# Kernel optimization log

Measured on AMD Instinct MI355X. Metric: run time of the kernel, lower is better.

The kernel has to match this reference:

```python
import jax, jax.numpy as jnp
import numpy as np

B, S, D, H = 4, 2048, 1024, 16
DK = D // H

def setup_inputs() -> dict:
    key = jax.random.key(0)
    ks = jax.random.split(key, 11)
    s = 1.0 / np.sqrt(D)
    return {
        "query": jax.random.normal(ks[0], (B, S, D), jnp.float32),
        "key_": jax.random.normal(ks[1], (B, S, D), jnp.float32),
        "value": jax.random.normal(ks[2], (B, S, D), jnp.float32),
        "Wq": jax.random.uniform(ks[3], (D, D), jnp.float32, -s, s),
        "bq": jax.random.uniform(ks[4], (D,), jnp.float32, -s, s),
        "Wk": jax.random.uniform(ks[5], (D, D), jnp.float32, -s, s),
        "bk": jax.random.uniform(ks[6], (D,), jnp.float32, -s, s),
        "Wv": jax.random.uniform(ks[7], (D, D), jnp.float32, -s, s),
        "bv": jax.random.uniform(ks[8], (D,), jnp.float32, -s, s),
        "Wo": jax.random.uniform(ks[9], (D, D), jnp.float32, -s, s),
        "bo": jax.random.uniform(ks[10], (D,), jnp.float32, -s, s),
    }

def _split_heads(x):
    # [B,S,D] -> [B,H,S,DK]
    b, s, _ = x.shape
    return x.reshape(b, s, H, DK).transpose(0, 2, 1, 3)

def reference(query, key_, value, Wq, bq, Wk, bk, Wv, bv, Wo, bo):
    Q = _split_heads(query @ Wq.T + bq)
    K = _split_heads(key_ @ Wk.T + bk)
    V = _split_heads(value @ Wv.T + bv)
    scores = jnp.einsum('bhqd,bhkd->bhqk', Q, K) / np.sqrt(DK).astype(np.float32)
    attn = jax.nn.softmax(scores, axis=-1)
    ctx = jnp.einsum('bhqk,bhkd->bhqd', attn, V)  # [B,H,S,DK]
    ctx = ctx.transpose(0, 2, 1, 3).reshape(query.shape[0], -1, D)
    return ctx @ Wo.T + bo
```

## Files before the change

kernel.cpp:

```cpp
#include <hip/hip_runtime.h>
#include <hip/hip_bf16.h>
#include <math.h>


#define B_SZ   4
#define S_LEN  2048
#define D_DIM  1024
#define NH     16
#define DKD    64
#define M_TOT  (B_SZ * S_LEN)

typedef __bf16 bf16_t;
typedef bf16_t bf16x8 __attribute__((ext_vector_type(8)));
typedef bf16_t bf16x4 __attribute__((ext_vector_type(4)));
typedef float  f32x4  __attribute__((ext_vector_type(4)));

typedef __attribute__((address_space(1))) void gvoid;
typedef __attribute__((address_space(3))) void lvoid;

extern "C" __device__ float __ocml_native_exp2_f32(float);

__global__ __launch_bounds__(256)
void cvt3_kernel(const float* __restrict__ s0, const float* __restrict__ s1,
                 const float* __restrict__ s2, bf16_t* __restrict__ d0,
                 bf16_t* __restrict__ d1, bf16_t* __restrict__ d2, int n4)
{
    const float* src = (blockIdx.z == 0) ? s0 : (blockIdx.z == 1) ? s1 : s2;
    bf16_t*      dst = (blockIdx.z == 0) ? d0 : (blockIdx.z == 1) ? d1 : d2;
    const int i = blockIdx.x * blockDim.x + threadIdx.x;
    if (i < n4) {
        f32x4 v = *(const f32x4*)(src + (size_t)i * 4);
        bf16x4 o;
        #pragma unroll
        for (int j = 0; j < 4; ++j) o[j] = (bf16_t)v[j];
        *(bf16x4*)(dst + (size_t)i * 4) = o;
    }
}

__global__ __launch_bounds__(256)
void cvt_kernel(const float* __restrict__ src, bf16_t* __restrict__ dst, int n4)
{
    const int i = blockIdx.x * blockDim.x + threadIdx.x;
    if (i < n4) {
        f32x4 v = *(const f32x4*)(src + (size_t)i * 4);
        bf16x4 o;
        #pragma unroll
        for (int j = 0; j < 4; ++j) o[j] = (bf16_t)v[j];
        *(bf16x4*)(dst + (size_t)i * 4) = o;
    }
}

__global__ __launch_bounds__(256, 3)
void qkv_gemm(const float* __restrict__ Aq, const float* __restrict__ Ak,
              const float* __restrict__ Av,
              const bf16_t* __restrict__ Wqb, const bf16_t* __restrict__ Wkb,
              const bf16_t* __restrict__ Wvb,
              const float* __restrict__ bq, const float* __restrict__ bk,
              const float* __restrict__ bv,
              bf16_t* __restrict__ Qw, bf16_t* __restrict__ Kw,
              bf16_t* __restrict__ Vt, float qscale)
{
    constexpr int K = 1024, N = 1024;
    constexpr int BM = 128, BK = 64;
    constexpr int NT = K / BK;

    __shared__ __align__(16) bf16_t lA[2][BM * 32];
    __shared__ __align__(16) bf16_t lB[2][2][128 * 32];

    const int z = blockIdx.z;
    const float* A  = (z == 0) ? Aq : (z == 1) ? Ak : Av;
    const bf16_t* W = (z == 0) ? Wqb : (z == 1) ? Wkb : Wvb;
    const float* bias = (z == 0) ? bq : (z == 1) ? bk : bv;
    const float scale = (z == 0) ? qscale : 1.0f;

    const int tid  = threadIdx.x;
    const int wave = tid >> 6;
    const int lane = tid & 63;

    const int row0 = blockIdx.x * BM;
    const int col0 = blockIdx.y * 128;

    const int wr = (wave >> 1) * 64;
    const int wc = (wave & 1) * 64;

    f32x4 acc[4][4] = {};

    const int frow = lane & 15;
    const int kq   = (lane >> 4) * 8;

    const int arow = tid >> 3;
    const int ak8  = (tid & 7) * 8;
    const int asub = (tid >> 2) & 1;
    const int akk  = (tid & 3) * 8;

    auto stageB = [&](int k0s, int bufi) {
        #pragma unroll
        for (int s = 0; s < 2; ++s)
            #pragma unroll
            for (int c2 = 0; c2 < 2; ++c2) {
                const int chunk = c2 * 4 + wave;
                const int e     = chunk * 512 + lane * 8;
                const int rr    = e >> 5;
                const int kk    = e & 31;
                __builtin_amdgcn_global_load_lds(
                    (gvoid*)(W + (size_t)(col0 + rr) * K + k0s + 32 * s + kk),
                    (lvoid*)(&lB[bufi][s][chunk * 512]), 16, 0, 0);
            }
    };

    stageB(0, 0);

    f32x4 pa[4][2];
    #pragma unroll
    for (int p = 0; p < 4; ++p) {
        const float* g = A + (size_t)(row0 + p * 32 + arow) * K + ak8;
        pa[p][0] = *(const f32x4*)g;
        pa[p][1] = *(const f32x4*)(g + 4);
    }

    for (int t = 0; t < NT; ++t) {
        const int k0  = t * BK;
        const int buf = t & 1;

        if (t + 1 < NT) stageB(k0 + BK, buf ^ 1);

        #pragma unroll
        for (int p = 0; p < 4; ++p) {
            bf16x8 a8;
            #pragma unroll
            for (int j = 0; j < 4; ++j) {
                a8[j]     = (bf16_t)pa[p][0][j];
                a8[4 + j] = (bf16_t)pa[p][1][j];
            }
            *(bf16x8*)(&lA[asub][(p * 32 + arow) * 32 + akk]) = a8;
        }

        if (t + 1 < NT)
            asm volatile("s_waitcnt vmcnt(4) lgkmcnt(0)" ::: "memory");
        else
            asm volatile("s_waitcnt vmcnt(0) lgkmcnt(0)" ::: "memory");
        __builtin_amdgcn_s_barrier();

        if (t + 1 < NT) {
            #pragma unroll
            for (int p = 0; p < 4; ++p) {
                const float* g = A + (size_t)(row0 + p * 32 + arow) * K + (k0 + BK) + ak8;
                pa[p][0] = *(const f32x4*)g;
                pa[p][1] = *(const f32x4*)(g + 4);
            }
        }

        #pragma unroll
        for (int s = 0; s < 2; ++s) {
            bf16x8 af[4], bfr[4];
            #pragma unroll
            for (int i = 0; i < 4; ++i) {
                af[i]  = *(const bf16x8*)(&lA[s][(wr + i * 16 + frow) * 32 + kq]);
                bfr[i] = *(const bf16x8*)(&lB[buf][s][(wc + i * 16 + frow) * 32 + kq]);
            }
            #pragma unroll
            for (int i = 0; i < 4; ++i)
                #pragma unroll
                for (int j = 0; j < 4; ++j)
                    acc[i][j] = __builtin_amdgcn_mfma_f32_16x16x32_bf16(af[i], bfr[j], acc[i][j], 0, 0, 0);
        }

        asm volatile("" ::: "memory");
        __builtin_amdgcn_s_barrier();
    }

    const int rb   = (lane >> 4) * 4;
    const int ccol = lane & 15;
    #pragma unroll
    for (int j = 0; j < 4; ++j) {
        const int n = col0 + wc + j * 16 + ccol;
        const float bvv = bias[n];
        #pragma unroll
        for (int i = 0; i < 4; ++i) {
            const int m = row0 + wr + i * 16 + rb;
            if (z == 2) {
                bf16x4 o4;
                #pragma unroll
                for (int r = 0; r < 4; ++r) o4[r] = (bf16_t)(acc[i][j][r] + bvv);
                *(bf16x4*)(Vt + (size_t)n * M_TOT + m) = o4;
            } else {
                bf16_t* Cp = (z == 0) ? Qw : Kw;
                #pragma unroll
                for (int r = 0; r < 4; ++r)
                    Cp[(size_t)(m + r) * N + n] = (bf16_t)((acc[i][j][r] + bvv) * scale);
            }
        }
    }
}

__global__ __launch_bounds__(256, 2)
void gemm_out(const bf16_t* __restrict__ A, const bf16_t* __restrict__ Bt,
              const float* __restrict__ bias, float* __restrict__ C)
{
    constexpr int K = 1024, N = 1024;
    constexpr int BM = 128, BK = 64;
    constexpr int NT = K / BK;

    __shared__ __align__(16) bf16_t lA[2][2][BM * 32];
    __shared__ __align__(16) bf16_t lB[2][2][128 * 32];

    const int tid  = threadIdx.x;
    const int wave = tid >> 6;
    const int lane = tid & 63;

    const int row0 = blockIdx.x * BM;
    const int col0 = blockIdx.y * 128;

    const int wr = (wave >> 1) * 64;
    const int wc = (wave & 1) * 64;

    f32x4 acc[4][4] = {};

    const int frow = lane & 15;
    const int kq   = (lane >> 4) * 8;

    auto stage = [&](int k0s, int bufi) {
        #pragma unroll
        for (int s = 0; s < 2; ++s)
            #pragma unroll
            for (int c2 = 0; c2 < 2; ++c2) {
                const int chunk = c2 * 4 + wave;
                const int e     = chunk * 512 + lane * 8;
                const int r     = e >> 5;
                const int kk    = e & 31;
                __builtin_amdgcn_global_load_lds(
                    (gvoid*)(A + (size_t)(row0 + r) * K + k0s + 32 * s + kk),
                    (lvoid*)(&lA[bufi][s][chunk * 512]), 16, 0, 0);
                __builtin_amdgcn_global_load_lds(
                    (gvoid*)(Bt + (size_t)(col0 + r) * K + k0s + 32 * s + kk),
                    (lvoid*)(&lB[bufi][s][chunk * 512]), 16, 0, 0);
            }
    };

    stage(0, 0);

    for (int t = 0; t < NT; ++t) {
        const int buf = t & 1;

        if (t + 1 < NT) {
            stage((t + 1) * BK, buf ^ 1);
            asm volatile("s_waitcnt vmcnt(8)" ::: "memory");
        } else {
            asm volatile("s_waitcnt vmcnt(0)" ::: "memory");
        }
        __builtin_amdgcn_s_barrier();

        #pragma unroll
        for (int s = 0; s < 2; ++s) {
            bf16x8 af[4], bfr[4];
            #pragma unroll
            for (int i = 0; i < 4; ++i) {
                af[i]  = *(const bf16x8*)(&lA[buf][s][(wr + i * 16 + frow) * 32 + kq]);
                bfr[i] = *(const bf16x8*)(&lB[buf][s][(wc + i * 16 + frow) * 32 + kq]);
            }
            #pragma unroll
            for (int i = 0; i < 4; ++i)
                #pragma unroll
                for (int j = 0; j < 4; ++j)
                    acc[i][j] = __builtin_amdgcn_mfma_f32_16x16x32_bf16(af[i], bfr[j], acc[i][j], 0, 0, 0);
        }

        asm volatile("" ::: "memory");
        __builtin_amdgcn_s_barrier();
    }

    const int rb   = (lane >> 4) * 4;
    const int ccol = lane & 15;
    #pragma unroll
    for (int j = 0; j < 4; ++j) {
        const int n = col0 + wc + j * 16 + ccol;
        const float bvv = bias[n];
        #pragma unroll
        for (int i = 0; i < 4; ++i) {
            const int m = row0 + wr + i * 16 + rb;
            #pragma unroll
            for (int r = 0; r < 4; ++r)
                C[(size_t)(m + r) * N + n] = acc[i][j][r] + bvv;
        }
    }
}

__global__ __launch_bounds__(256, 2)
void attn_mfma(const bf16_t* __restrict__ Qg, const bf16_t* __restrict__ Kg,
               const bf16_t* __restrict__ Vt, bf16_t* __restrict__ ctx)
{
    constexpr int PSTR = 72;
    __shared__ __align__(16) bf16_t lK[64 * PSTR];
    __shared__ __align__(16) bf16_t lV[64 * PSTR];
    __shared__ __align__(16) bf16_t lP[4][64 * PSTR];

    const int tid  = threadIdx.x;
    const int wave = tid >> 6;
    const int lane = tid & 63;
    const int qd   = lane >> 4;
    const int c    = lane & 15;

    const int g    = blockIdx.x;
    const int bh   = ((g >> 6) << 3) | (g & 7);
    const int qblk = (g >> 3) & 7;
    const int b    = bh >> 4;
    const int h    = bh & 15;

    const int q0 = qblk * 256 + wave * 64;

    const bf16_t* Qb = Qg + ((size_t)(b * S_LEN + q0)) * D_DIM + h * DKD;
    const bf16_t* Kb = Kg + ((size_t)(b * S_LEN)) * D_DIM + h * DKD;
    const bf16_t* Vb = Vt + ((size_t)(h * DKD)) * M_TOT + b * S_LEN;

    bf16_t* Pw = &lP[wave][0];

    bf16x8 qf[4][2];
    #pragma unroll
    for (int qt = 0; qt < 4; ++qt)
        #pragma unroll
        for (int ks = 0; ks < 2; ++ks)
            qf[qt][ks] = *(const bf16x8*)(Qb + (size_t)(qt * 16 + c) * D_DIM + ks * 32 + qd * 8);

    bf16x8 ones;
    #pragma unroll
    for (int i = 0; i < 8; ++i) ones[i] = (bf16_t)1.0f;

    f32x4 oacc[4][4] = {};
    f32x4 lacc[4]    = {};

    const int srow = tid >> 3;
    const int sc8  = (tid & 7) * 8;

    bf16x8 kv[2], vv[2];
    #pragma unroll
    for (int cc = 0; cc < 2; ++cc) {
        const int row = cc * 32 + srow;
        kv[cc] = *(const bf16x8*)(Kb + (size_t)row * D_DIM + sc8);
        vv[cc] = *(const bf16x8*)(Vb + (size_t)row * M_TOT + sc8);
    }

    for (int kt = 0; kt < S_LEN; kt += 64) {
        __syncthreads();
        #pragma unroll
        for (int cc = 0; cc < 2; ++cc) {
            const int row = cc * 32 + srow;
            *(bf16x8*)(lK + row * PSTR + sc8) = kv[cc];
            *(bf16x8*)(lV + row * PSTR + sc8) = vv[cc];
        }
        __syncthreads();

        if (kt + 64 < S_LEN) {
            #pragma unroll
            for (int cc = 0; cc < 2; ++cc) {
                const int row = cc * 32 + srow;
                kv[cc] = *(const bf16x8*)(Kb + (size_t)(kt + 64 + row) * D_DIM + sc8);
                vv[cc] = *(const bf16x8*)(Vb + (size_t)row * M_TOT + kt + 64 + sc8);
            }
        }

        bf16x8 kf[4][2];
        #pragma unroll
        for (int i = 0; i < 4; ++i)
            #pragma unroll
            for (int ks = 0; ks < 2; ++ks)
                kf[i][ks] = *(const bf16x8*)(lK + (i * 16 + c) * PSTR + ks * 32 + qd * 8);

        #pragma unroll
        for (int qh = 0; qh < 2; ++qh) {
            f32x4 st[4][2] = {};
            __builtin_amdgcn_s_setprio(1);
            #pragma unroll
            for (int ks = 0; ks < 2; ++ks)
                #pragma unroll
                for (int i = 0; i < 4; ++i)
                    #pragma unroll
                    for (int qt = 0; qt < 2; ++qt)
                        st[i][qt] = __builtin_amdgcn_mfma_f32_16x16x32_bf16(
                            kf[i][ks], qf[qh * 2 + qt][ks], st[i][qt], 0, 0, 0);
            __builtin_amdgcn_s_setprio(0);

            #pragma unroll
            for (int i = 0; i < 4; ++i)
                #pragma unroll
                for (int qt = 0; qt < 2; ++qt) {
                    bf16x4 pw;
                    #pragma unroll
                    for (int r = 0; r < 4; ++r)
                        pw[r] = (bf16_t)__ocml_native_exp2_f32(st[i][qt][r]);
                    *(bf16x4*)(Pw + ((qh * 2 + qt) * 16 + c) * PSTR + i * 16 + qd * 4) = pw;
                }
        }

        bf16x8 vf[4][2];
        #pragma unroll
        for (int fm = 0; fm < 4; ++fm)
            #pragma unroll
            for (int ks = 0; ks < 2; ++ks)
                vf[fm][ks] = *(const bf16x8*)(lV + (fm * 16 + c) * PSTR + ks * 32 + qd * 8);

        __builtin_amdgcn_s_setprio(1);
        #pragma unroll
        for (int qn = 0; qn < 4; ++qn)
            #pragma unroll
            for (int ks = 0; ks < 2; ++ks) {
                bf16x8 pf = *(const bf16x8*)(Pw + (qn * 16 + c) * PSTR + ks * 32 + qd * 8);
                lacc[qn] = __builtin_amdgcn_mfma_f32_16x16x32_bf16(ones, pf, lacc[qn], 0, 0, 0);
                #pragma unroll
                for (int fm = 0; fm < 4; ++fm)
                    oacc[fm][qn] = __builtin_amdgcn_mfma_f32_16x16x32_bf16(vf[fm][ks], pf, oacc[fm][qn], 0, 0, 0);
            }
        __builtin_amdgcn_s_setprio(0);
    }

    #pragma unroll
    for (int qn = 0; qn < 4; ++qn) {
        const float linv = 1.0f / lacc[qn][0];
        bf16_t* op = ctx + ((size_t)(b * S_LEN + q0 + qn * 16 + c)) * D_DIM + h * DKD + qd * 4;
        #pragma unroll
        for (int fm = 0; fm < 4; ++fm) {
            bf16x4 o4;
            #pragma unroll
            for (int r = 0; r < 4; ++r) o4[r] = (bf16_t)(oacc[fm][qn][r] * linv);
            *(bf16x4*)(op + fm * 16) = o4;
        }
    }
}

extern "C" void kernel_launch(void* const* d_in, const int* in_sizes, int n_in,
                              void* d_out, int out_size, void* d_ws, size_t ws_size,
                              hipStream_t stream)
{
    const float* query = (const float*)d_in[0];
    const float* key_  = (const float*)d_in[1];
    const float* value = (const float*)d_in[2];
    const float* Wq    = (const float*)d_in[3];
    const float* bq    = (const float*)d_in[4];
    const float* Wk    = (const float*)d_in[5];
    const float* bk    = (const float*)d_in[6];
    const float* Wv    = (const float*)d_in[7];
    const float* bv    = (const float*)d_in[8];
    const float* Wo    = (const float*)d_in[9];
    const float* bo    = (const float*)d_in[10];
    float* out = (float*)d_out;

    const size_t mat  = (size_t)M_TOT * D_DIM;
    const size_t wmat = (size_t)D_DIM * D_DIM;

    bf16_t* t0 = (bf16_t*)d_ws;
    bf16_t* w0 = t0 + mat;
    bf16_t* Qw = w0 + wmat;
    bf16_t* Kw = Qw + mat;
    bf16_t* Vt = Kw + mat;
    bf16_t* w1 = t0;
    bf16_t* w2 = t0 + wmat;

    const int gcvt_w = (int)(wmat / 4 / 256);
    const float qscale = 0.18033688011112042f;

    cvt3_kernel<<<dim3(gcvt_w, 1, 3), 256, 0, stream>>>(Wq, Wk, Wv, w0, w1, w2,
                                                        (int)(wmat / 4));

    qkv_gemm<<<dim3(M_TOT / 128, D_DIM / 128, 3), 256, 0, stream>>>(
        query, key_, value, w0, w1, w2, bq, bk, bv, Qw, Kw, Vt, qscale);

    cvt_kernel<<<gcvt_w, 256, 0, stream>>>(Wo, w0, (int)(wmat / 4));

    attn_mfma<<<dim3(B_SZ * NH * (S_LEN / 256)), 256, 0, stream>>>(Qw, Kw, Vt, t0);

    gemm_out<<<dim3(M_TOT / 128, D_DIM / 128), 256, 0, stream>>>(t0, w0, bo, out);
}
```

Measured before the change: 330.9 us.

## Shrink output GEMM tile to 64 rows and drop LDS double buffering

The output projection GEMM changes from 128x128 tiles to 64x128 tiles and doubles the grid. The double-buffered global_load_lds pipeline becomes a single-buffered loop with __syncthreads around each K step. Occupancy rises to four blocks per CU through launch bounds and smaller LDS use. The cost is that load latency is no longer overlapped with MFMA, and each tile reuses B data across fewer rows.

```diff
diff --git a/kernel.cpp b/kernel.cpp
--- a/kernel.cpp
+++ b/kernel.cpp
@@ -193,16 +193,15 @@
     }
 }
 
-__global__ __launch_bounds__(256, 2)
+__global__ __launch_bounds__(256, 4)
 void gemm_out(const bf16_t* __restrict__ A, const bf16_t* __restrict__ Bt,
               const float* __restrict__ bias, float* __restrict__ C)
 {
     constexpr int K = 1024, N = 1024;
-    constexpr int BM = 128, BK = 64;
-    constexpr int NT = K / BK;
-
-    __shared__ __align__(16) bf16_t lA[2][2][BM * 32];
-    __shared__ __align__(16) bf16_t lB[2][2][128 * 32];
+    constexpr int BM = 64, BK = 64;
+
+    __shared__ __align__(16) bf16_t lA[2][BM * 32];
+    __shared__ __align__(16) bf16_t lB[2][128 * 32];
 
     const int tid  = threadIdx.x;
     const int wave = tid >> 6;
@@ -211,17 +210,26 @@
     const int row0 = blockIdx.x * BM;
     const int col0 = blockIdx.y * 128;
 
-    const int wr = (wave >> 1) * 64;
+    const int wr = (wave >> 1) * 32;
     const int wc = (wave & 1) * 64;
 
-    f32x4 acc[4][4] = {};
+    f32x4 acc[2][4] = {};
 
     const int frow = lane & 15;
     const int kq   = (lane >> 4) * 8;
 
-    auto stage = [&](int k0s, int bufi) {
-        #pragma unroll
-        for (int s = 0; s < 2; ++s)
+    for (int k0 = 0; k0 < K; k0 += BK) {
+        __syncthreads();
+        #pragma unroll
+        for (int s = 0; s < 2; ++s) {
+            {
+                const int e  = wave * 512 + lane * 8;
+                const int r  = e >> 5;
+                const int kk = e & 31;
+                __builtin_amdgcn_global_load_lds(
+                    (gvoid*)(A + (size_t)(row0 + r) * K + k0 + 32 * s + kk),
+                    (lvoid*)(&lA[s][wave * 512]), 16, 0, 0);
+            }
             #pragma unroll
             for (int c2 = 0; c2 < 2; ++c2) {
                 const int chunk = c2 * 4 + wave;
@@ -229,44 +237,27 @@
                 const int r     = e >> 5;
                 const int kk    = e & 31;
                 __builtin_amdgcn_global_load_lds(
-                    (gvoid*)(A + (size_t)(row0 + r) * K + k0s + 32 * s + kk),
-                    (lvoid*)(&lA[bufi][s][chunk * 512]), 16, 0, 0);
-                __builtin_amdgcn_global_load_lds(
-                    (gvoid*)(Bt + (size_t)(col0 + r) * K + k0s + 32 * s + kk),
-                    (lvoid*)(&lB[bufi][s][chunk * 512]), 16, 0, 0);
-            }
-    };
-
-    stage(0, 0);
-
-    for (int t = 0; t < NT; ++t) {
-        const int buf = t & 1;
-
-        if (t + 1 < NT) {
-            stage((t + 1) * BK, buf ^ 1);
-            asm volatile("s_waitcnt vmcnt(8)" ::: "memory");
-        } else {
-            asm volatile("s_waitcnt vmcnt(0)" ::: "memory");
-        }
-        __builtin_amdgcn_s_barrier();
+                    (gvoid*)(Bt + (size_t)(col0 + r) * K + k0 + 32 * s + kk),
+                    (lvoid*)(&lB[s][chunk * 512]), 16, 0, 0);
+            }
+        }
+        __syncthreads();
 
         #pragma unroll
         for (int s = 0; s < 2; ++s) {
-            bf16x8 af[4], bfr[4];
-            #pragma unroll
-            for (int i = 0; i < 4; ++i) {
-                af[i]  = *(const bf16x8*)(&lA[buf][s][(wr + i * 16 + frow) * 32 + kq]);
-                bfr[i] = *(const bf16x8*)(&lB[buf][s][(wc + i * 16 + frow) * 32 + kq]);
-            }
-            #pragma unroll
-            for (int i = 0; i < 4; ++i)
+            bf16x8 af[2], bfr[4];
+            #pragma unroll
+            for (int i = 0; i < 2; ++i)
+                af[i] = *(const bf16x8*)(&lA[s][(wr + i * 16 + frow) * 32 + kq]);
+            #pragma unroll
+            for (int j = 0; j < 4; ++j)
+                bfr[j] = *(const bf16x8*)(&lB[s][(wc + j * 16 + frow) * 32 + kq]);
+            #pragma unroll
+            for (int i = 0; i < 2; ++i)
                 #pragma unroll
                 for (int j = 0; j < 4; ++j)
                     acc[i][j] = __builtin_amdgcn_mfma_f32_16x16x32_bf16(af[i], bfr[j], acc[i][j], 0, 0, 0);
         }
-
-        asm volatile("" ::: "memory");
-        __builtin_amdgcn_s_barrier();
     }
 
     const int rb   = (lane >> 4) * 4;
@@ -276,7 +267,7 @@
         const int n = col0 + wc + j * 16 + ccol;
         const float bvv = bias[n];
         #pragma unroll
-        for (int i = 0; i < 4; ++i) {
+        for (int i = 0; i < 2; ++i) {
             const int m = row0 + wr + i * 16 + rb;
             #pragma unroll
             for (int r = 0; r < 4; ++r)
@@ -467,5 +458,5 @@
 
     attn_mfma<<<dim3(B_SZ * NH * (S_LEN / 256)), 256, 0, stream>>>(Qw, Kw, Vt, t0);
 
-    gemm_out<<<dim3(M_TOT / 128, D_DIM / 128), 256, 0, stream>>>(t0, w0, bo, out);
-}
+    gemm_out<<<dim3(M_TOT / 64, D_DIM / 128), 256, 0, stream>>>(t0, w0, bo, out);
+}
```

Result: slower. 339.2 us (+2.5%).

## Stage fp32 activations directly into LDS via async loads and convert at fragment read

Applied to the files above, without the earlier changes.

The QKV projection GEMM now loads fp32 activation tiles straight into LDS with global_load_lds, using an XOR swizzle to avoid bank conflicts, instead of loading them into registers and converting to bf16 before the LDS store. Conversion to bf16 moves to the point where MFMA fragments are read from LDS. The K tile shrinks from 64 to 32 so the fp32 A tile fits the LDS budget. This removes the register round-trip and the conversion stall from the load path, but doubles the number of k-iterations and barriers and doubles LDS read traffic for A.

```diff
diff --git a/kernel.cpp b/kernel.cpp
--- a/kernel.cpp
+++ b/kernel.cpp
@@ -61,11 +61,11 @@
               bf16_t* __restrict__ Vt, float qscale)
 {
     constexpr int K = 1024, N = 1024;
-    constexpr int BM = 128, BK = 64;
+    constexpr int BM = 128, BK = 32;
     constexpr int NT = K / BK;
 
-    __shared__ __align__(16) bf16_t lA[2][BM * 32];
-    __shared__ __align__(16) bf16_t lB[2][2][128 * 32];
+    __shared__ __align__(16) float  lAf[2][BM * 32];
+    __shared__ __align__(16) bf16_t lB [2][128 * 32];
 
     const int z = blockIdx.z;
     const float* A  = (z == 0) ? Aq : (z == 1) ? Ak : Av;
@@ -88,82 +88,60 @@
     const int frow = lane & 15;
     const int kq   = (lane >> 4) * 8;
 
-    const int arow = tid >> 3;
-    const int ak8  = (tid & 7) * 8;
-    const int asub = (tid >> 2) & 1;
-    const int akk  = (tid & 3) * 8;
-
-    auto stageB = [&](int k0s, int bufi) {
-        #pragma unroll
-        for (int s = 0; s < 2; ++s)
-            #pragma unroll
-            for (int c2 = 0; c2 < 2; ++c2) {
-                const int chunk = c2 * 4 + wave;
-                const int e     = chunk * 512 + lane * 8;
-                const int rr    = e >> 5;
-                const int kk    = e & 31;
-                __builtin_amdgcn_global_load_lds(
-                    (gvoid*)(W + (size_t)(col0 + rr) * K + k0s + 32 * s + kk),
-                    (lvoid*)(&lB[bufi][s][chunk * 512]), 16, 0, 0);
-            }
+    auto stage = [&](int k0s, int bufi) {
+        #pragma unroll
+        for (int c2 = 0; c2 < 4; ++c2) {
+            const int chunk = c2 * 4 + wave;
+            const int rr    = chunk * 8 + (lane >> 3);
+            const int kk    = ((lane & 7) ^ (rr & 7)) * 4;
+            __builtin_amdgcn_global_load_lds(
+                (gvoid*)(A + (size_t)(row0 + rr) * K + k0s + kk),
+                (lvoid*)(&lAf[bufi][chunk * 256]), 16, 0, 0);
+        }
+        #pragma unroll
+        for (int c2 = 0; c2 < 2; ++c2) {
+            const int chunk = c2 * 4 + wave;
+            const int rr    = chunk * 16 + (lane >> 2);
+            const int kk    = (lane & 3) * 8;
+            __builtin_amdgcn_global_load_lds(
+                (gvoid*)(W + (size_t)(col0 + rr) * K + k0s + kk),
+                (lvoid*)(&lB[bufi][chunk * 512]), 16, 0, 0);
+        }
     };
 
-    stageB(0, 0);
-
-    f32x4 pa[4][2];
-    #pragma unroll
-    for (int p = 0; p < 4; ++p) {
-        const float* g = A + (size_t)(row0 + p * 32 + arow) * K + ak8;
-        pa[p][0] = *(const f32x4*)g;
-        pa[p][1] = *(const f32x4*)(g + 4);
-    }
+    stage(0, 0);
 
     for (int t = 0; t < NT; ++t) {
-        const int k0  = t * BK;
         const int buf = t & 1;
 
-        if (t + 1 < NT) stageB(k0 + BK, buf ^ 1);
-
-        #pragma unroll
-        for (int p = 0; p < 4; ++p) {
-            bf16x8 a8;
-            #pragma unroll
-            for (int j = 0; j < 4; ++j) {
-                a8[j]     = (bf16_t)pa[p][0][j];
-                a8[4 + j] = (bf16_t)pa[p][1][j];
-            }
-            *(bf16x8*)(&lA[asub][(p * 32 + arow) * 32 + akk]) = a8;
-        }
-
-        if (t + 1 < NT)
-            asm volatile("s_waitcnt vmcnt(4) lgkmcnt(0)" ::: "memory");
-        else
-            asm volatile("s_waitcnt vmcnt(0) lgkmcnt(0)" ::: "memory");
+        if (t + 1 < NT) {
+            stage((t + 1) * BK, buf ^ 1);
+            asm volatile("s_waitcnt vmcnt(6)" ::: "memory");
+        } else {
+            asm volatile("s_waitcnt vmcnt(0)" ::: "memory");
+        }
         __builtin_amdgcn_s_barrier();
 
-        if (t + 1 < NT) {
-            #pragma unroll
-            for (int p = 0; p < 4; ++p) {
-                const float* g = A + (size_t)(row0 + p * 32 + arow) * K + (k0 + BK) + ak8;
-                pa[p][0] = *(const f32x4*)g;
-                pa[p][1] = *(const f32x4*)(g + 4);
-            }
-        }
-
-        #pragma unroll
-        for (int s = 0; s < 2; ++s) {
-            bf16x8 af[4], bfr[4];
-            #pragma unroll
-            for (int i = 0; i < 4; ++i) {
-                af[i]  = *(const bf16x8*)(&lA[s][(wr + i * 16 + frow) * 32 + kq]);
-                bfr[i] = *(const bf16x8*)(&lB[buf][s][(wc + i * 16 + frow) * 32 + kq]);
-            }
-            #pragma unroll
-            for (int i = 0; i < 4; ++i)
-                #pragma unroll
-                for (int j = 0; j < 4; ++j)
-                    acc[i][j] = __builtin_amdgcn_mfma_f32_16x16x32_bf16(af[i], bfr[j], acc[i][j], 0, 0, 0);
-        }
+        const float* Ab = &lAf[buf][0];
+        bf16x8 af[4], bfr[4];
+        #pragma unroll
+        for (int i = 0; i < 4; ++i) {
+            const int r = wr + i * 16 + frow;
+            const int m = (r & 7) * 4;
+            f32x4 lo = *(const f32x4*)(Ab + r * 32 + (kq ^ m));
+            f32x4 hi = *(const f32x4*)(Ab + r * 32 + ((kq + 4) ^ m));
+            #pragma unroll
+            for (int jj = 0; jj < 4; ++jj) {
+                af[i][jj]     = (bf16_t)lo[jj];
+                af[i][4 + jj] = (bf16_t)hi[jj];
+            }
+            bfr[i] = *(const bf16x8*)(&lB[buf][(wc + i * 16 + frow) * 32 + kq]);
+        }
+        #pragma unroll
+        for (int i = 0; i < 4; ++i)
+            #pragma unroll
+            for (int j = 0; j < 4; ++j)
+                acc[i][j] = __builtin_amdgcn_mfma_f32_16x16x32_bf16(af[i], bfr[j], acc[i][j], 0, 0, 0);
 
         asm volatile("" ::: "memory");
         __builtin_amdgcn_s_barrier();
```

New measurement: 343.2 us. 1.04x slower.

## Widen GEMM tiles to 128x256 with 8 waves, swizzle LDS, prioritize MFMA

Applied to the files above, without the earlier changes.

Both projection GEMMs now use 512-thread blocks computing 128x256 output tiles, so each staged A tile is reused across twice as many columns and fewer blocks are launched. LDS layouts gain an XOR swizzle on the k-chunk index, applied consistently on the store side and the fragment-read side, to reduce bank conflicts. s_setprio is raised around the MFMA bursts. The cost is more LDS per block, fewer blocks in the grid, and a reworked wait count that has to match the new number of outstanding loads.

```diff
diff --git a/kernel.cpp b/kernel.cpp
--- a/kernel.cpp
+++ b/kernel.cpp
@@ -50,7 +50,7 @@
     }
 }
 
-__global__ __launch_bounds__(256, 3)
+__global__ __launch_bounds__(512, 2)
 void qkv_gemm(const float* __restrict__ Aq, const float* __restrict__ Ak,
               const float* __restrict__ Av,
               const bf16_t* __restrict__ Wqb, const bf16_t* __restrict__ Wkb,
@@ -61,11 +61,11 @@
               bf16_t* __restrict__ Vt, float qscale)
 {
     constexpr int K = 1024, N = 1024;
-    constexpr int BM = 128, BK = 64;
+    constexpr int BK = 64;
     constexpr int NT = K / BK;
 
-    __shared__ __align__(16) bf16_t lA[2][BM * 32];
-    __shared__ __align__(16) bf16_t lB[2][2][128 * 32];
+    __shared__ __align__(16) bf16_t lA[2][128 * 32];
+    __shared__ __align__(16) bf16_t lB[2][2][256 * 32];
 
     const int z = blockIdx.z;
     const float* A  = (z == 0) ? Aq : (z == 1) ? Ak : Av;
@@ -77,31 +77,30 @@
     const int wave = tid >> 6;
     const int lane = tid & 63;
 
-    const int row0 = blockIdx.x * BM;
-    const int col0 = blockIdx.y * 128;
-
-    const int wr = (wave >> 1) * 64;
-    const int wc = (wave & 1) * 64;
+    const int row0 = blockIdx.x * 128;
+    const int col0 = blockIdx.y * 256;
+
+    const int wr = (wave >> 2) * 64;
+    const int wc = (wave & 3) * 64;
 
     f32x4 acc[4][4] = {};
 
     const int frow = lane & 15;
-    const int kq   = (lane >> 4) * 8;
+    const int kqs = (((lane >> 4) ^ ((frow >> 1) & 3))) * 8;
 
     const int arow = tid >> 3;
     const int ak8  = (tid & 7) * 8;
     const int asub = (tid >> 2) & 1;
-    const int akk  = (tid & 3) * 8;
+    const int akks = (((tid & 3) ^ ((tid >> 4) & 3))) * 8;
 
     auto stageB = [&](int k0s, int bufi) {
         #pragma unroll
         for (int s = 0; s < 2; ++s)
             #pragma unroll
             for (int c2 = 0; c2 < 2; ++c2) {
-                const int chunk = c2 * 4 + wave;
-                const int e     = chunk * 512 + lane * 8;
-                const int rr    = e >> 5;
-                const int kk    = e & 31;
+                const int chunk = c2 * 8 + wave;
+                const int rr    = chunk * 16 + (lane >> 2);
+                const int kk    = (((lane & 3) ^ ((lane >> 3) & 3))) * 8;
                 __builtin_amdgcn_global_load_lds(
                     (gvoid*)(W + (size_t)(col0 + rr) * K + k0s + 32 * s + kk),
                     (lvoid*)(&lB[bufi][s][chunk * 512]), 16, 0, 0);
@@ -110,10 +109,10 @@
 
     stageB(0, 0);
 
-    f32x4 pa[4][2];
-    #pragma unroll
-    for (int p = 0; p < 4; ++p) {
-        const float* g = A + (size_t)(row0 + p * 32 + arow) * K + ak8;
+    f32x4 pa[2][2];
+    #pragma unroll
+    for (int p = 0; p < 2; ++p) {
+        const float* g = A + (size_t)(row0 + p * 64 + arow) * K + ak8;
         pa[p][0] = *(const f32x4*)g;
         pa[p][1] = *(const f32x4*)(g + 4);
     }
@@ -125,14 +124,14 @@
         if (t + 1 < NT) stageB(k0 + BK, buf ^ 1);
 
         #pragma unroll
-        for (int p = 0; p < 4; ++p) {
+        for (int p = 0; p < 2; ++p) {
             bf16x8 a8;
             #pragma unroll
             for (int j = 0; j < 4; ++j) {
                 a8[j]     = (bf16_t)pa[p][0][j];
                 a8[4 + j] = (bf16_t)pa[p][1][j];
             }
-            *(bf16x8*)(&lA[asub][(p * 32 + arow) * 32 + akk]) = a8;
+            *(bf16x8*)(&lA[asub][(p * 64 + arow) * 32 + akks]) = a8;
         }
 
         if (t + 1 < NT)
@@ -143,8 +142,8 @@
 
         if (t + 1 < NT) {
             #pragma unroll
-            for (int p = 0; p < 4; ++p) {
-                const float* g = A + (size_t)(row0 + p * 32 + arow) * K + (k0 + BK) + ak8;
+            for (int p = 0; p < 2; ++p) {
+                const float* g = A + (size_t)(row0 + p * 64 + arow) * K + (k0 + BK) + ak8;
                 pa[p][0] = *(const f32x4*)g;
                 pa[p][1] = *(const f32x4*)(g + 4);
             }
@@ -155,14 +154,16 @@
             bf16x8 af[4], bfr[4];
             #pragma unroll
             for (int i = 0; i < 4; ++i) {
-                af[i]  = *(const bf16x8*)(&lA[s][(wr + i * 16 + frow) * 32 + kq]);
-                bfr[i] = *(const bf16x8*)(&lB[buf][s][(wc + i * 16 + frow) * 32 + kq]);
-            }
+                af[i]  = *(const bf16x8*)(&lA[s][(wr + i * 16 + frow) * 32 + kqs]);
+                bfr[i] = *(const bf16x8*)(&lB[buf][s][(wc + i * 16 + frow) * 32 + kqs]);
+            }
+            __builtin_amdgcn_s_setprio(1);
             #pragma unroll
             for (int i = 0; i < 4; ++i)
                 #pragma unroll
                 for (int j = 0; j < 4; ++j)
                     acc[i][j] = __builtin_amdgcn_mfma_f32_16x16x32_bf16(af[i], bfr[j], acc[i][j], 0, 0, 0);
+            __builtin_amdgcn_s_setprio(0);
         }
 
         asm volatile("" ::: "memory");
@@ -193,48 +194,52 @@
     }
 }
 
-__global__ __launch_bounds__(256, 2)
+__global__ __launch_bounds__(512, 2)
 void gemm_out(const bf16_t* __restrict__ A, const bf16_t* __restrict__ Bt,
               const float* __restrict__ bias, float* __restrict__ C)
 {
     constexpr int K = 1024, N = 1024;
-    constexpr int BM = 128, BK = 64;
+    constexpr int BK = 64;
     constexpr int NT = K / BK;
 
-    __shared__ __align__(16) bf16_t lA[2][2][BM * 32];
-    __shared__ __align__(16) bf16_t lB[2][2][128 * 32];
+    __shared__ __align__(16) bf16_t lA[2][2][128 * 32];
+    __shared__ __align__(16) bf16_t lB[2][2][256 * 32];
 
     const int tid  = threadIdx.x;
     const int wave = tid >> 6;
     const int lane = tid & 63;
 
-    const int row0 = blockIdx.x * BM;
-    const int col0 = blockIdx.y * 128;
-
-    const int wr = (wave >> 1) * 64;
-    const int wc = (wave & 1) * 64;
+    const int row0 = blockIdx.x * 128;
+    const int col0 = blockIdx.y * 256;
+
+    const int wr = (wave >> 2) * 64;
+    const int wc = (wave & 3) * 64;
 
     f32x4 acc[4][4] = {};
 
     const int frow = lane & 15;
-    const int kq   = (lane >> 4) * 8;
+    const int kqs  = (((lane >> 4) ^ ((frow >> 1) & 3))) * 8;
 
     auto stage = [&](int k0s, int bufi) {
-        #pragma unroll
-        for (int s = 0; s < 2; ++s)
+        const int kk = (((lane & 3) ^ ((lane >> 3) & 3))) * 8;
+        #pragma unroll
+        for (int s = 0; s < 2; ++s) {
+            {
+                const int chunk = wave;
+                const int rr    = chunk * 16 + (lane >> 2);
+                __builtin_amdgcn_global_load_lds(
+                    (gvoid*)(A + (size_t)(row0 + rr) * K + k0s + 32 * s + kk),
+                    (lvoid*)(&lA[bufi][s][chunk * 512]), 16, 0, 0);
+            }
             #pragma unroll
             for (int c2 = 0; c2 < 2; ++c2) {
-                const int chunk = c2 * 4 + wave;
-                const int e     = chunk * 512 + lane * 8;
-                const int r     = e >> 5;
-                const int kk    = e & 31;
+                const int chunk = c2 * 8 + wave;
+                const int rr    = chunk * 16 + (lane >> 2);
                 __builtin_amdgcn_global_load_lds(
-                    (gvoid*)(A + (size_t)(row0 + r) * K + k0s + 32 * s + kk),
-                    (lvoid*)(&lA[bufi][s][chunk * 512]), 16, 0, 0);
-                __builtin_amdgcn_global_load_lds(
-                    (gvoid*)(Bt + (size_t)(col0 + r) * K + k0s + 32 * s + kk),
+                    (gvoid*)(Bt + (size_t)(col0 + rr) * K + k0s + 32 * s + kk),
                     (lvoid*)(&lB[bufi][s][chunk * 512]), 16, 0, 0);
             }
+        }
     };
 
     stage(0, 0);
@@ -244,7 +249,7 @@
 
         if (t + 1 < NT) {
             stage((t + 1) * BK, buf ^ 1);
-            asm volatile("s_waitcnt vmcnt(8)" ::: "memory");
+            asm volatile("s_waitcnt vmcnt(6)" ::: "memory");
         } else {
             asm volatile("s_waitcnt vmcnt(0)" ::: "memory");
         }
@@ -255,14 +260,16 @@
             bf16x8 af[4], bfr[4];
             #pragma unroll
             for (int i = 0; i < 4; ++i) {
-                af[i]  = *(const bf16x8*)(&lA[buf][s][(wr + i * 16 + frow) * 32 + kq]);
-                bfr[i] = *(const bf16x8*)(&lB[buf][s][(wc + i * 16 + frow) * 32 + kq]);
-            }
+                af[i]  = *(const bf16x8*)(&lA[buf][s][(wr + i * 16 + frow) * 32 + kqs]);
+                bfr[i] = *(const bf16x8*)(&lB[buf][s][(wc + i * 16 + frow) * 32 + kqs]);
+            }
+            __builtin_amdgcn_s_setprio(1);
             #pragma unroll
             for (int i = 0; i < 4; ++i)
                 #pragma unroll
                 for (int j = 0; j < 4; ++j)
                     acc[i][j] = __builtin_amdgcn_mfma_f32_16x16x32_bf16(af[i], bfr[j], acc[i][j], 0, 0, 0);
+            __builtin_amdgcn_s_setprio(0);
         }
 
         asm volatile("" ::: "memory");
@@ -460,12 +467,12 @@
     cvt3_kernel<<<dim3(gcvt_w, 1, 3), 256, 0, stream>>>(Wq, Wk, Wv, w0, w1, w2,
                                                         (int)(wmat / 4));
 
-    qkv_gemm<<<dim3(M_TOT / 128, D_DIM / 128, 3), 256, 0, stream>>>(
+    qkv_gemm<<<dim3(M_TOT / 128, D_DIM / 256, 3), 512, 0, stream>>>(
         query, key_, value, w0, w1, w2, bq, bk, bv, Qw, Kw, Vt, qscale);
 
     cvt_kernel<<<gcvt_w, 256, 0, stream>>>(Wo, w0, (int)(wmat / 4));
 
     attn_mfma<<<dim3(B_SZ * NH * (S_LEN / 256)), 256, 0, stream>>>(Qw, Kw, Vt, t0);
 
-    gemm_out<<<dim3(M_TOT / 128, D_DIM / 128), 256, 0, stream>>>(t0, w0, bo, out);
-}
+    gemm_out<<<dim3(M_TOT / 128, D_DIM / 256), 512, 0, stream>>>(t0, w0, bo, out);
+}
```

After: 341.2 us. +3.1%, slower.
